# Kernel tuning notes

Hardware: AMD Instinct MI355X
Metric: run time of the kernel (lower is better)

## Reference

```python
import jax, jax.numpy as jnp
import numpy as np

N_NODES = 100000
N_EDGES = 625000
D = 128


def setup_inputs() -> dict:
    key = jax.random.key(0)
    ks = jax.random.split(key, 6)
    x = jax.random.normal(ks[0], (N_NODES, D), dtype=jnp.float32)
    src = jax.random.randint(ks[1], (N_EDGES,), 0, N_NODES, dtype=jnp.int32)
    dst = jnp.sort(jax.random.randint(ks[2], (N_EDGES,), 0, N_NODES, dtype=jnp.int32))
    edge_w = jax.random.uniform(ks[3], (N_EDGES,), dtype=jnp.float32)
    # linear layer params (fan-in scaled)
    W = jax.random.normal(ks[4], (D, D), dtype=jnp.float32) / np.sqrt(D)
    b = jnp.zeros((D,), dtype=jnp.float32)
    # highway gate params (glorot-uniform-ish range as in source)
    init_range = np.sqrt(2.0 / (D + D)).astype(np.float32)
    kernel_gate = jax.random.uniform(ks[5], (D, D), dtype=jnp.float32,
                                     minval=-init_range, maxval=init_range)
    bias_gate = jnp.zeros((D,), dtype=jnp.float32)
    return {"x": x, "src": src, "dst": dst, "edge_w": edge_w,
            "W": W, "b": b, "kernel_gate": kernel_gate, "bias_gate": bias_gate}


def reference(x, src, dst, edge_w, W, b, kernel_gate, bias_gate):
    # hidden = Linear(x); dropout is identity in eval mode
    hidden = x @ W.T + b                                  # [N, D]
    # support = spmm(adj, hidden): gather src rows, weight, scatter-add to dst
    msgs = edge_w[:, None] * hidden[src]                  # [E, D]
    support = jax.ops.segment_sum(msgs, dst, num_segments=x.shape[0])
    support = jax.nn.relu(support)                        # act
    # highway gate
    gate = jax.nn.sigmoid(x @ kernel_gate + bias_gate)    # [N, D]
    out = gate * support + (1.0 - gate) * x
    return out
```

## Files before the change

### kernel.cpp

```cpp
#include <hip/hip_runtime.h>

#define DD 128

typedef __attribute__((ext_vector_type(8))) short bf16x8;
typedef __attribute__((ext_vector_type(4))) float f32x4;

__device__ __forceinline__ unsigned int cvt_pk_bf16(float lo, float hi) {
  unsigned int r;
  asm("v_cvt_pk_bf16_f32 %0, %1, %2" : "=v"(r) : "v"(lo), "v"(hi));
  return r;
}
__device__ __forceinline__ float bf_lo(unsigned int v) { return __uint_as_float(v << 16); }
__device__ __forceinline__ float bf_hi(unsigned int v) { return __uint_as_float(v & 0xFFFF0000u); }

__global__ __launch_bounds__(256) void prep_kernel(
    const float* __restrict__ x, const int* __restrict__ dst,
    const float* __restrict__ W, const float* __restrict__ KG,
    unsigned char* __restrict__ xq, float* __restrict__ sx,
    int* __restrict__ row_start, unsigned short* __restrict__ B,
    int N, int E, int ABLK, int BBLK) {
  int blk = blockIdx.x;
  int t = threadIdx.x;
  if (blk < ABLK) {
    int n = blk * 16 + (t >> 4);
    int lr = t & 15;
    if (n < N) {
      const float4* xr = (const float4*)(x + (size_t)n * DD);
      float4 va = xr[lr * 2], vb = xr[lr * 2 + 1];
      float m = fmaxf(fmaxf(fmaxf(fabsf(va.x), fabsf(va.y)), fmaxf(fabsf(va.z), fabsf(va.w))),
                      fmaxf(fmaxf(fabsf(vb.x), fabsf(vb.y)), fmaxf(fabsf(vb.z), fabsf(vb.w))));
#pragma unroll
      for (int d = 1; d < 16; d <<= 1) m = fmaxf(m, __shfl_xor(m, d, 16));
      m = fmaxf(m, 1e-20f);
      float inv = 127.0f / m;
      unsigned int q0 = (unsigned int)(__float2int_rn(va.x * inv) + 128);
      unsigned int q1 = (unsigned int)(__float2int_rn(va.y * inv) + 128);
      unsigned int q2 = (unsigned int)(__float2int_rn(va.z * inv) + 128);
      unsigned int q3 = (unsigned int)(__float2int_rn(va.w * inv) + 128);
      unsigned int q4 = (unsigned int)(__float2int_rn(vb.x * inv) + 128);
      unsigned int q5 = (unsigned int)(__float2int_rn(vb.y * inv) + 128);
      unsigned int q6 = (unsigned int)(__float2int_rn(vb.z * inv) + 128);
      unsigned int q7 = (unsigned int)(__float2int_rn(vb.w * inv) + 128);
      uint2 qp;
      qp.x = q0 | (q1 << 8) | (q2 << 16) | (q3 << 24);
      qp.y = q4 | (q5 << 8) | (q6 << 16) | (q7 << 24);
      ((uint2*)xq)[(size_t)n * 16 + lr] = qp;
      if (lr == 0) sx[n] = m * (1.0f / 127.0f);
    }
  } else if (blk < ABLK + BBLK) {
    int e = (blk - ABLK) * 256 + t;
    if (e <= E) {
      if (e == 0) {
        int d0 = dst[0];
        for (int n = 0; n <= d0; ++n) row_start[n] = 0;
      } else if (e == E) {
        for (int n = dst[E - 1] + 1; n <= N; ++n) row_start[n] = E;
      } else {
        int d = dst[e], dp = dst[e - 1];
        for (int n = dp + 1; n <= d; ++n) row_start[n] = e;
      }
    }
  } else {
    int e2 = (blk - ABLK - BBLK) * 256 + t;
    if (e2 < 2 * DD * DD) {
      int j = e2 >> 7, k = e2 & 127;
      float v = (j < DD) ? W[j * DD + k] : KG[k * DD + (j - DD)];
      B[e2] = (unsigned short)cvt_pk_bf16(v, v);
    }
  }
}

__global__ __launch_bounds__(256, 8) void scatter_agg(
    const unsigned char* __restrict__ xq, const float* __restrict__ sx,
    const int* __restrict__ src, const float* __restrict__ ew,
    const int* __restrict__ row_start, unsigned short* __restrict__ aggb,
    float* __restrict__ sumw, int N, int E) {
  int t = threadIdx.x;
  int wid = t >> 6, lane = t & 63;
  int g = lane >> 4, lr = lane & 15;
  int n = blockIdx.x * 16 + wid * 4 + g;
  bool valid = (n < N);
  int b = valid ? row_start[n] : 0;
  int cnt = valid ? (row_start[n + 1] - b) : 0;
  const uint2* x8 = (const uint2*)xq;

  float a[8];
#pragma unroll
  for (int k = 0; k < 8; ++k) a[k] = 0.f;
  float wsum = 0.f, wsc = 0.f;
  int clampj = cnt > 0 ? cnt - 1 : 0;

  int i = 0;
  while (__any(i < cnt)) {
#pragma unroll
    for (int u = 0; u < 4; ++u) {
      int ii = i + u;
      int jj = ii < clampj ? ii : clampj;
      int j = b + jj;
      if (j > E - 1) j = E - 1;
      float wt = (ii < cnt) ? ew[j] : 0.f;
      int s = src[j];
      float ws = wt * sx[s];
      uint2 v = x8[(size_t)s * 16 + lr];
      wsum += wt;
      wsc += ws;
      a[0] += ws * (float)(v.x & 0xFF);
      a[1] += ws * (float)((v.x >> 8) & 0xFF);
      a[2] += ws * (float)((v.x >> 16) & 0xFF);
      a[3] += ws * (float)(v.x >> 24);
      a[4] += ws * (float)(v.y & 0xFF);
      a[5] += ws * (float)((v.y >> 8) & 0xFF);
      a[6] += ws * (float)((v.y >> 16) & 0xFF);
      a[7] += ws * (float)(v.y >> 24);
    }
    i += 4;
  }
  float c = 128.0f * wsc;
#pragma unroll
  for (int k = 0; k < 8; ++k) a[k] -= c;

  if (valid) {
    uint4 o;
    o.x = cvt_pk_bf16(a[0], a[1]);
    o.y = cvt_pk_bf16(a[2], a[3]);
    o.z = cvt_pk_bf16(a[4], a[5]);
    o.w = cvt_pk_bf16(a[6], a[7]);
    ((uint4*)aggb)[(size_t)n * 16 + lr] = o;
    if (lr == 0) sumw[n] = wsum;
  }
}

__global__ __launch_bounds__(256, 3) void fused_gemm(
    const unsigned char* __restrict__ xq, const float* __restrict__ sx,
    const unsigned short* __restrict__ aggb, const unsigned short* __restrict__ B,
    const float* __restrict__ sumw, const float* __restrict__ bias,
    const float* __restrict__ bg, float* __restrict__ out, int N) {
  __shared__ char smem[32 * 1024];
  unsigned short* sX = (unsigned short*)smem;
  unsigned short* sA = (unsigned short*)(smem + 16384);
  int t = threadIdx.x;
  int wid = t >> 6, lane = t & 63;
  int lr = lane & 15, lk2 = lane >> 4;
  int jw = wid * 32;
  int M0 = blockIdx.x * 64;

  bf16x8 wS[4][2], wG[4][2];
#pragma unroll
  for (int kc = 0; kc < 4; ++kc)
#pragma unroll
    for (int m = 0; m < 2; ++m) {
      int j = jw + m * 16 + lr;
      wS[kc][m] = *(const bf16x8*)(B + (size_t)j * DD + kc * 32 + lk2 * 8);
      wG[kc][m] = *(const bf16x8*)(B + (size_t)(DD + j) * DD + kc * 32 + lk2 * 8);
    }

#pragma unroll
  for (int i = 0; i < 2; ++i) {
    int idx = i * 256 + t;
    int r = idx >> 3;
    int c = idx & 7;
    uint4 v;
    float s;
    if (M0 + r < N) {
      v = ((const uint4*)(xq + (size_t)(M0 + r) * DD))[c];
      s = sx[M0 + r];
    } else {
      v = make_uint4(0, 0, 0, 0);
      s = 0.f;
    }
    float nb = -128.0f * s;
    unsigned int w[4] = {v.x, v.y, v.z, v.w};
    unsigned int o[8];
#pragma unroll
    for (int q = 0; q < 4; ++q) {
      float e0 = fmaf(s, (float)(w[q] & 0xFF), nb);
      float e1 = fmaf(s, (float)((w[q] >> 8) & 0xFF), nb);
      float e2 = fmaf(s, (float)((w[q] >> 16) & 0xFF), nb);
      float e3 = fmaf(s, (float)(w[q] >> 24), nb);
      o[q * 2]     = cvt_pk_bf16(e0, e1);
      o[q * 2 + 1] = cvt_pk_bf16(e2, e3);
    }
    int base = r * 256 + c * 32;
    uint4 lo = {o[0], o[1], o[2], o[3]};
    uint4 hi = {o[4], o[5], o[6], o[7]};
    *(uint4*)((char*)sX + ((base) ^ ((r & 7) << 4)))      = lo;
    *(uint4*)((char*)sX + ((base + 16) ^ ((r & 7) << 4))) = hi;
  }
#pragma unroll
  for (int i = 0; i < 4; ++i) {
    int idx = i * 256 + t;
    int r = idx >> 4, c = idx & 15;
    uint4 va;
    if (M0 + r < N) va = ((const uint4*)(aggb + (size_t)(M0 + r) * DD))[c];
    else            va = make_uint4(0, 0, 0, 0);
    int off = (r * 256 + c * 16) ^ ((r & 7) << 4);
    *(uint4*)((char*)sA + off) = va;
  }
  __syncthreads();

  f32x4 accS[2][4], accG[2][4];
#pragma unroll
  for (int m = 0; m < 2; ++m)
#pragma unroll
    for (int nr = 0; nr < 4; ++nr) {
      accS[m][nr] = (f32x4){0.f, 0.f, 0.f, 0.f};
      accG[m][nr] = (f32x4){0.f, 0.f, 0.f, 0.f};
    }

#pragma unroll
  for (int kc = 0; kc < 4; ++kc) {
    int kb = (kc * 32 + lk2 * 8) * 2;
    bf16x8 af[4], xf[4];
#pragma unroll
    for (int nr = 0; nr < 4; ++nr) {
      int r = nr * 16 + lr;
      int off = (r * 256 + kb) ^ ((r & 7) << 4);
      af[nr] = *(const bf16x8*)((const char*)sA + off);
      xf[nr] = *(const bf16x8*)((const char*)sX + off);
    }
#pragma unroll
    for (int m = 0; m < 2; ++m)
#pragma unroll
      for (int nr = 0; nr < 4; ++nr) {
        accS[m][nr] = __builtin_amdgcn_mfma_f32_16x16x32_bf16(wS[kc][m], af[nr], accS[m][nr], 0, 0, 0);
        accG[m][nr] = __builtin_amdgcn_mfma_f32_16x16x32_bf16(wG[kc][m], xf[nr], accG[m][nr], 0, 0, 0);
      }
  }

#pragma unroll
  for (int m = 0; m < 2; ++m) {
    int j0 = jw + m * 16 + lk2 * 4;
    float4 b4 = *(const float4*)&bias[j0];
    float4 bg4 = *(const float4*)&bg[j0];
    float ba[4] = {b4.x, b4.y, b4.z, b4.w};
    float bga[4] = {bg4.x, bg4.y, bg4.z, bg4.w};
#pragma unroll
    for (int nr = 0; nr < 4; ++nr) {
      int node = M0 + nr * 16 + lr;
      if (node < N) {
        float sw = sumw[node];
        int r = nr * 16 + lr;
        uint2 qx = *(const uint2*)((const char*)sX + ((r * 256 + j0 * 2) ^ ((r & 7) << 4)));
        float xr[4] = {bf_lo(qx.x), bf_hi(qx.x), bf_lo(qx.y), bf_hi(qx.y)};
        f32x4 vs = accS[m][nr], vg = accG[m][nr];
        float4 o;
        float* op = &o.x;
#pragma unroll
        for (int reg = 0; reg < 4; ++reg) {
          float s = fmaxf(vs[reg] + sw * ba[reg], 0.f);
          float g = 1.0f / (1.0f + __expf(-(vg[reg] + bga[reg])));
          op[reg] = g * s + (1.0f - g) * xr[reg];
        }
        *(float4*)&out[(size_t)node * DD + j0] = o;
      }
    }
  }
}

extern "C" void kernel_launch(void* const* d_in, const int* in_sizes, int n_in,
                              void* d_out, int out_size, void* d_ws, size_t ws_size,
                              hipStream_t stream) {
  const float* x   = (const float*)d_in[0];
  const int*   src = (const int*)d_in[1];
  const int*   dst = (const int*)d_in[2];
  const float* ew  = (const float*)d_in[3];
  const float* W   = (const float*)d_in[4];
  const float* b   = (const float*)d_in[5];
  const float* KG  = (const float*)d_in[6];
  const float* bg  = (const float*)d_in[7];
  float* out = (float*)d_out;

  int N = in_sizes[0] / DD;
  int E = in_sizes[1];

  unsigned short* aggb = (unsigned short*)d_ws;
  unsigned char* xq = (unsigned char*)(aggb + (size_t)N * DD);
  float* sx = (float*)(xq + (size_t)N * DD);
  float* sumw = sx + N;
  unsigned short* B = (unsigned short*)(sumw + N);
  int* row_start = (int*)(B + 2 * DD * DD);

  int ABLK = (N + 15) / 16;
  int BBLK = (E + 1 + 255) / 256;
  int CBLK = (2 * DD * DD + 255) / 256;
  prep_kernel<<<ABLK + BBLK + CBLK, 256, 0, stream>>>(x, dst, W, KG, xq, sx,
                                                      row_start, B, N, E, ABLK, BBLK);
  scatter_agg<<<(N + 15) / 16, 256, 0, stream>>>(xq, sx, src, ew, row_start, aggb, sumw, N, E);
  fused_gemm<<<(N + 63) / 64, 256, 0, stream>>>(xq, sx, aggb, B, sumw, b, bg, out, N);
}
```

Measured before the change: 77.68 us.

## Precompute per-edge scaled weights in a separate kernel and unroll gather by 8

Adds an edge_prep kernel that computes ew*sx[src] per edge and the per-node weight sums. This removes the dependent sx[s] gather and the wsum accumulation from the scatter aggregation loop. The aggregation loop unroll also goes from 4 to 8 to keep more gathers in flight. The cost is an extra kernel launch, an extra E-sized write and read, and a serial per-node loop that recomputes the weight sums.

Result: slower. 85.00 us (+9.4%).

```diff
diff --git a/kernel.cpp b/kernel.cpp
--- a/kernel.cpp
+++ b/kernel.cpp
@@ -70,11 +70,31 @@
   }
 }
 
+__global__ __launch_bounds__(256) void edge_prep(
+    const int* __restrict__ src, const float* __restrict__ ew,
+    const float* __restrict__ sx, const int* __restrict__ row_start,
+    float* __restrict__ ews, float* __restrict__ sumw,
+    int N, int E, int EBLK) {
+  int blk = blockIdx.x;
+  int t = threadIdx.x;
+  if (blk < EBLK) {
+    int e = blk * 256 + t;
+    if (e < E) ews[e] = ew[e] * sx[src[e]];
+  } else {
+    int n = (blk - EBLK) * 256 + t;
+    if (n < N) {
+      int b = row_start[n], en = row_start[n + 1];
+      float s = 0.f;
+      for (int j = b; j < en; ++j) s += ew[j];
+      sumw[n] = s;
+    }
+  }
+}
+
 __global__ __launch_bounds__(256, 8) void scatter_agg(
-    const unsigned char* __restrict__ xq, const float* __restrict__ sx,
-    const int* __restrict__ src, const float* __restrict__ ew,
-    const int* __restrict__ row_start, unsigned short* __restrict__ aggb,
-    float* __restrict__ sumw, int N, int E) {
+    const unsigned char* __restrict__ xq, const int* __restrict__ src,
+    const float* __restrict__ ews, const int* __restrict__ row_start,
+    unsigned short* __restrict__ aggb, int N, int E) {
   int t = threadIdx.x;
   int wid = t >> 6, lane = t & 63;
   int g = lane >> 4, lr = lane & 15;
@@ -87,33 +107,31 @@
   float a[8];
 #pragma unroll
   for (int k = 0; k < 8; ++k) a[k] = 0.f;
-  float wsum = 0.f, wsc = 0.f;
+  float wsc = 0.f;
   int clampj = cnt > 0 ? cnt - 1 : 0;
 
   int i = 0;
   while (__any(i < cnt)) {
 #pragma unroll
-    for (int u = 0; u < 4; ++u) {
+    for (int u = 0; u < 8; ++u) {
       int ii = i + u;
       int jj = ii < clampj ? ii : clampj;
       int j = b + jj;
       if (j > E - 1) j = E - 1;
-      float wt = (ii < cnt) ? ew[j] : 0.f;
+      float wt = (ii < cnt) ? ews[j] : 0.f;
       int s = src[j];
-      float ws = wt * sx[s];
       uint2 v = x8[(size_t)s * 16 + lr];
-      wsum += wt;
-      wsc += ws;
-      a[0] += ws * (float)(v.x & 0xFF);
-      a[1] += ws * (float)((v.x >> 8) & 0xFF);
-      a[2] += ws * (float)((v.x >> 16) & 0xFF);
-      a[3] += ws * (float)(v.x >> 24);
-      a[4] += ws * (float)(v.y & 0xFF);
-      a[5] += ws * (float)((v.y >> 8) & 0xFF);
-      a[6] += ws * (float)((v.y >> 16) & 0xFF);
-      a[7] += ws * (float)(v.y >> 24);
-    }
-    i += 4;
+      wsc += wt;
+      a[0] += wt * (float)(v.x & 0xFF);
+      a[1] += wt * (float)((v.x >> 8) & 0xFF);
+      a[2] += wt * (float)((v.x >> 16) & 0xFF);
+      a[3] += wt * (float)(v.x >> 24);
+      a[4] += wt * (float)(v.y & 0xFF);
+      a[5] += wt * (float)((v.y >> 8) & 0xFF);
+      a[6] += wt * (float)((v.y >> 16) & 0xFF);
+      a[7] += wt * (float)(v.y >> 24);
+    }
+    i += 8;
   }
   float c = 128.0f * wsc;
 #pragma unroll
@@ -126,7 +144,6 @@
     o.z = cvt_pk_bf16(a[4], a[5]);
     o.w = cvt_pk_bf16(a[6], a[7]);
     ((uint4*)aggb)[(size_t)n * 16 + lr] = o;
-    if (lr == 0) sumw[n] = wsum;
   }
 }
 
@@ -277,14 +294,18 @@
   unsigned char* xq = (unsigned char*)(aggb + (size_t)N * DD);
   float* sx = (float*)(xq + (size_t)N * DD);
   float* sumw = sx + N;
-  unsigned short* B = (unsigned short*)(sumw + N);
+  float* ews = sumw + N;
+  unsigned short* B = (unsigned short*)(ews + E);
   int* row_start = (int*)(B + 2 * DD * DD);
 
   int ABLK = (N + 15) / 16;
   int BBLK = (E + 1 + 255) / 256;
   int CBLK = (2 * DD * DD + 255) / 256;
+  int EBLK = (E + 255) / 256;
+  int NBLK = (N + 255) / 256;
   prep_kernel<<<ABLK + BBLK + CBLK, 256, 0, stream>>>(x, dst, W, KG, xq, sx,
                                                       row_start, B, N, E, ABLK, BBLK);
-  scatter_agg<<<(N + 15) / 16, 256, 0, stream>>>(xq, sx, src, ew, row_start, aggb, sumw, N, E);
+  edge_prep<<<EBLK + NBLK, 256, 0, stream>>>(src, ew, sx, row_start, ews, sumw, N, E, EBLK);
+  scatter_agg<<<(N + 15) / 16, 256, 0, stream>>>(xq, src, ews, row_start, aggb, N, E);
   fused_gemm<<<(N + 63) / 64, 256, 0, stream>>>(xq, sx, aggb, B, sumw, b, bg, out, N);
 }
```

## Load aggregated rows directly from global and stream weights per k-chunk

Applied to the files above, without the earlier changes.

The fused GEMM no longer stages the aggregated bf16 tile in shared memory. Each lane reads its MFMA fragments straight from global memory, and the weight fragments are loaded inside each k-chunk instead of being held in registers for the whole kernel. Together with halving LDS and raising the launch-bounds occupancy hint from 3 to 4, this aims to cut register and LDS pressure so more blocks fit per CU. In exchange, the MFMA loop now waits on global-load latency and re-reads weights from cache on every chunk.

Result: slower. 83.12 us (+7.0%).

```diff
diff --git a/kernel.cpp b/kernel.cpp
--- a/kernel.cpp
+++ b/kernel.cpp
@@ -130,29 +130,18 @@
   }
 }
 
-__global__ __launch_bounds__(256, 3) void fused_gemm(
+__global__ __launch_bounds__(256, 4) void fused_gemm(
     const unsigned char* __restrict__ xq, const float* __restrict__ sx,
     const unsigned short* __restrict__ aggb, const unsigned short* __restrict__ B,
     const float* __restrict__ sumw, const float* __restrict__ bias,
     const float* __restrict__ bg, float* __restrict__ out, int N) {
-  __shared__ char smem[32 * 1024];
+  __shared__ char smem[16 * 1024];
   unsigned short* sX = (unsigned short*)smem;
-  unsigned short* sA = (unsigned short*)(smem + 16384);
   int t = threadIdx.x;
   int wid = t >> 6, lane = t & 63;
   int lr = lane & 15, lk2 = lane >> 4;
   int jw = wid * 32;
   int M0 = blockIdx.x * 64;
-
-  bf16x8 wS[4][2], wG[4][2];
-#pragma unroll
-  for (int kc = 0; kc < 4; ++kc)
-#pragma unroll
-    for (int m = 0; m < 2; ++m) {
-      int j = jw + m * 16 + lr;
-      wS[kc][m] = *(const bf16x8*)(B + (size_t)j * DD + kc * 32 + lk2 * 8);
-      wG[kc][m] = *(const bf16x8*)(B + (size_t)(DD + j) * DD + kc * 32 + lk2 * 8);
-    }
 
 #pragma unroll
   for (int i = 0; i < 2; ++i) {
@@ -186,17 +175,15 @@
     *(uint4*)((char*)sX + ((base) ^ ((r & 7) << 4)))      = lo;
     *(uint4*)((char*)sX + ((base + 16) ^ ((r & 7) << 4))) = hi;
   }
-#pragma unroll
-  for (int i = 0; i < 4; ++i) {
-    int idx = i * 256 + t;
-    int r = idx >> 4, c = idx & 15;
-    uint4 va;
-    if (M0 + r < N) va = ((const uint4*)(aggb + (size_t)(M0 + r) * DD))[c];
-    else            va = make_uint4(0, 0, 0, 0);
-    int off = (r * 256 + c * 16) ^ ((r & 7) << 4);
-    *(uint4*)((char*)sA + off) = va;
-  }
   __syncthreads();
+
+  const unsigned short* arow[4];
+#pragma unroll
+  for (int nr = 0; nr < 4; ++nr) {
+    int node = M0 + nr * 16 + lr;
+    if (node > N - 1) node = N - 1;
+    arow[nr] = aggb + (size_t)node * DD;
+  }
 
   f32x4 accS[2][4], accG[2][4];
 #pragma unroll
@@ -210,20 +197,26 @@
 #pragma unroll
   for (int kc = 0; kc < 4; ++kc) {
     int kb = (kc * 32 + lk2 * 8) * 2;
+    bf16x8 wSk[2], wGk[2];
+#pragma unroll
+    for (int m = 0; m < 2; ++m) {
+      int j = jw + m * 16 + lr;
+      wSk[m] = *(const bf16x8*)(B + (size_t)j * DD + kc * 32 + lk2 * 8);
+      wGk[m] = *(const bf16x8*)(B + (size_t)(DD + j) * DD + kc * 32 + lk2 * 8);
+    }
     bf16x8 af[4], xf[4];
 #pragma unroll
     for (int nr = 0; nr < 4; ++nr) {
+      af[nr] = *(const bf16x8*)(arow[nr] + kc * 32 + lk2 * 8);
       int r = nr * 16 + lr;
-      int off = (r * 256 + kb) ^ ((r & 7) << 4);
-      af[nr] = *(const bf16x8*)((const char*)sA + off);
-      xf[nr] = *(const bf16x8*)((const char*)sX + off);
+      xf[nr] = *(const bf16x8*)((const char*)sX + ((r * 256 + kb) ^ ((r & 7) << 4)));
     }
 #pragma unroll
     for (int m = 0; m < 2; ++m)
 #pragma unroll
       for (int nr = 0; nr < 4; ++nr) {
-        accS[m][nr] = __builtin_amdgcn_mfma_f32_16x16x32_bf16(wS[kc][m], af[nr], accS[m][nr], 0, 0, 0);
-        accG[m][nr] = __builtin_amdgcn_mfma_f32_16x16x32_bf16(wG[kc][m], xf[nr], accG[m][nr], 0, 0, 0);
+        accS[m][nr] = __builtin_amdgcn_mfma_f32_16x16x32_bf16(wSk[m], af[nr], accS[m][nr], 0, 0, 0);
+        accG[m][nr] = __builtin_amdgcn_mfma_f32_16x16x32_bf16(wGk[m], xf[nr], accG[m][nr], 0, 0, 0);
       }
   }
 
```
